# Optimization experiments

Measured on AMD Instinct MI355X. Metric: run time of the kernel, lower is better.

Reference implementation:

```python
import jax, jax.numpy as jnp
import numpy as np

N_NODES = 50000
N_EDGES = 800000
IN_FT = 256
OUT_FT = 128


def setup_inputs() -> dict:
    key = jax.random.key(0)
    k_seq, k_src, k_dst, k_val, k_w = jax.random.split(key, 5)
    seq = jax.random.normal(k_seq, (N_NODES, IN_FT), dtype=jnp.float32)
    edge_src = jax.random.randint(k_src, (N_EDGES,), 0, N_NODES, dtype=jnp.int64)
    edge_dst = jax.random.randint(k_dst, (N_EDGES,), 0, N_NODES, dtype=jnp.int64)
    edge_val = jax.random.uniform(k_val, (N_EDGES,), dtype=jnp.float32)
    # xavier_uniform for Linear(in_ft, out_ft): limit = sqrt(6/(in+out))
    limit = float(np.sqrt(6.0 / (IN_FT + OUT_FT)))
    W = jax.random.uniform(k_w, (OUT_FT, IN_FT), minval=-limit, maxval=limit, dtype=jnp.float32)
    bias = jnp.zeros((OUT_FT,), dtype=jnp.float32)
    prelu_a = jnp.full((1,), 0.25, dtype=jnp.float32)  # nn.PReLU default slope
    return {"seq": seq, "edge_src": edge_src, "edge_dst": edge_dst,
            "edge_val": edge_val, "W": W, "bias": bias, "prelu_a": prelu_a}


def reference(seq, edge_src, edge_dst, edge_val, W, bias, prelu_a):
    # seq_fts = fc(seq): [N, out_ft]
    seq_fts = jnp.einsum('ni,oi->no', seq, W)
    # sparse spmm: out[dst] += val * seq_fts[src]
    msgs = seq_fts[edge_src] * edge_val[:, None]          # [E, out_ft]
    out = jax.ops.segment_sum(msgs, edge_dst, num_segments=seq.shape[0])
    out = out + bias                                       # bias add
    # PReLU with learnable slope a
    return jnp.where(out >= 0, out, prelu_a * out)
```

## Files before the change

kernel.cpp:

```cpp
#include <hip/hip_runtime.h>
#include <hip/hip_bf16.h>

#define N_NODES 50000
#define N_EDGES 800000
#define IN_FT 256
#define OUT_FT 128

typedef __bf16 bf16;
typedef __attribute__((ext_vector_type(8))) __bf16 bf16x8;
typedef __attribute__((ext_vector_type(4))) __bf16 bf16x4;
typedef __attribute__((ext_vector_type(4))) float floatx4;

static __device__ inline unsigned short f2bf_bits(float f) {
    unsigned u = __float_as_uint(f);
    return (unsigned short)((u + 0x7FFFu + ((u >> 16) & 1u)) >> 16);
}

#define BKN 128
#define NBUCK 392
#define EPB 2048
#define NBLK_A ((N_EDGES + EPB - 1) / EPB)
#define CELL 32
#define SXCAP 2560
#define GM 128
#define GEMM_BLKS ((N_NODES + GM - 1) / GM)
#define WP 264
#define OP 136
#define SMEM_BYTES (128 * OP * 2 > 64 * WP * 2 ? 128 * OP * 2 : 64 * WP * 2)

template<int NTHREADS>
__device__ inline int blk_scan_incl(int v, int t, int* wsum) {
    const int lane = t & 63;
    const int w = t >> 6;
#pragma unroll
    for (int s = 1; s < 64; s <<= 1) {
        int o = __shfl_up(v, s, 64);
        if (lane >= s) v += o;
    }
    __syncthreads();
    if (lane == 63) wsum[w] = v;
    __syncthreads();
    if (w == 0) {
        constexpr int NWAVE = NTHREADS / 64;
        int x = (lane < NWAVE) ? wsum[lane] : 0;
#pragma unroll
        for (int s = 1; s < NWAVE; s <<= 1) {
            int o = __shfl_up(x, s, 64);
            if (lane >= s) x += o;
        }
        if (lane < NWAVE) wsum[lane] = x;
    }
    __syncthreads();
    return v + ((w > 0) ? wsum[w - 1] : 0);
}

__global__ __launch_bounds__(512, 6) void k_ga(const float* __restrict__ seq,
                                               const float* __restrict__ W,
                                               unsigned short* __restrict__ seq_fts,
                                               const int* __restrict__ src,
                                               const int* __restrict__ dst,
                                               const float* __restrict__ val,
                                               int* __restrict__ cnt,
                                               uint2* __restrict__ part) {
    const int t = threadIdx.x;
    __shared__ __align__(16) char smem[SMEM_BYTES];
    if (blockIdx.x < GEMM_BLKS) {
        bf16* Wlds = (bf16*)smem;
        const int lane = t & 63;
        const int wave = t >> 6;
        const int quad = lane >> 4;
        const int l16  = lane & 15;

        int arow = blockIdx.x * GM + wave * 16 + l16;
        if (arow >= N_NODES) arow = 0;
        const float* ap = seq + (size_t)arow * IN_FT + quad * 8;
        bf16x8 afr[8];
#pragma unroll
        for (int s = 0; s < 8; ++s) {
            float4 v0 = *(const float4*)(ap + s * 32);
            float4 v1 = *(const float4*)(ap + s * 32 + 4);
            bf16x8 a;
            a[0] = (bf16)v0.x; a[1] = (bf16)v0.y; a[2] = (bf16)v0.z; a[3] = (bf16)v0.w;
            a[4] = (bf16)v1.x; a[5] = (bf16)v1.y; a[6] = (bf16)v1.z; a[7] = (bf16)v1.w;
            afr[s] = a;
        }

        floatx4 acc[2][4];
#pragma unroll
        for (int h2 = 0; h2 < 2; ++h2)
#pragma unroll
            for (int q = 0; q < 4; ++q) acc[h2][q] = (floatx4){0.f, 0.f, 0.f, 0.f};

#pragma unroll
        for (int h2 = 0; h2 < 2; ++h2) {
            __syncthreads();
            {
                const int row = t >> 3;
                const int c0 = (t & 7) * 32;
                const float* wsrc = W + (size_t)(h2 * 64 + row) * IN_FT + c0;
                bf16* dstp = Wlds + row * WP + c0;
#pragma unroll
                for (int c = 0; c < 8; ++c) {
                    float4 vv = *(const float4*)(wsrc + c * 4);
                    bf16x4 o = {(bf16)vv.x, (bf16)vv.y, (bf16)vv.z, (bf16)vv.w};
                    *(bf16x4*)(dstp + c * 4) = o;
                }
            }
            __syncthreads();
#pragma unroll
            for (int s = 0; s < 8; ++s) {
#pragma unroll
                for (int q = 0; q < 4; ++q) {
                    bf16x8 bfr = *(const bf16x8*)(Wlds + (q * 16 + l16) * WP + quad * 8 + s * 32);
                    acc[h2][q] = __builtin_amdgcn_mfma_f32_16x16x32_bf16(afr[s], bfr, acc[h2][q], 0, 0, 0);
                }
            }
        }
        __syncthreads();
        unsigned short* olds = (unsigned short*)smem;
#pragma unroll
        for (int h2 = 0; h2 < 2; ++h2)
#pragma unroll
            for (int q = 0; q < 4; ++q) {
                const int col = (h2 * 4 + q) * 16 + l16;
#pragma unroll
                for (int r = 0; r < 4; ++r)
                    olds[(wave * 16 + quad * 4 + r) * OP + col] = f2bf_bits(acc[h2][q][r]);
            }
        __syncthreads();
        {
            const int lr0 = t >> 4;
            const int cseg = (t & 15) * 8;
            const int mb = blockIdx.x * GM;
#pragma unroll
            for (int it = 0; it < 4; ++it) {
                const int lr = it * 32 + lr0;
                const int m = mb + lr;
                if (m < N_NODES)
                    *(uint4*)(seq_fts + (size_t)m * OUT_FT + cseg) =
                        *(const uint4*)(olds + lr * OP + cseg);
            }
        }
    } else {
        int*   ib    = (int*)smem;
        int*   h     = ib;
        int*   lbase = ib + 392;
        int*   wsum  = ib + 784;
        int*   totp  = ib + 792;
        uint2* srt   = (uint2*)(smem + 3200);

        const int B2 = blockIdx.x - GEMM_BLKS;
        const int e0 = B2 * EPB;
        if (t < NBUCK) h[t] = 0;
        __syncthreads();

        int      myd[4];
        int      myofs[4];
        unsigned myx[4];
#pragma unroll
        for (int k = 0; k < 4; ++k) {
            int e = e0 + k * 512 + t;
            int d = (e < N_EDGES) ? dst[e] : -1;
            myd[k] = d;
            if (d >= 0) {
                myx[k] = (unsigned)(unsigned short)src[e]
                       | ((unsigned)f2bf_bits(val[e]) << 16);
                myofs[k] = atomicAdd(&h[d >> 7], 1);
            }
        }
        __syncthreads();
        const int v = (t < NBUCK) ? min(h[t], CELL) : 0;
        const int inc = blk_scan_incl<512>(v, t, wsum);
        if (t < NBUCK) { lbase[t] = inc - v; cnt[t * NBLK_A + B2] = v; }
        if (t == 511) *totp = inc;
        __syncthreads();
        const int total = *totp;
#pragma unroll
        for (int k = 0; k < 4; ++k) {
            int d = myd[k];
            if (d >= 0 && myofs[k] < CELL)
                srt[lbase[d >> 7] + myofs[k]] = make_uint2(myx[k], (unsigned)d);
        }
        __syncthreads();
        for (int i = t; i < total; i += 512) {
            uint2 r = srt[i];
            int bb = (int)(r.y >> 7);
            part[(size_t)(bb * NBLK_A + B2) * CELL + (unsigned)(i - lbase[bb])] = r;
        }
    }
}

#define NW 16
__global__ __launch_bounds__(1024) void k_BG(const int* __restrict__ cnt,
                                             const uint2* __restrict__ part,
                                             const unsigned* __restrict__ fts,
                                             const float* __restrict__ bias,
                                             const float* __restrict__ prelu_a,
                                             float* __restrict__ out) {
    const int b = blockIdx.x, t = threadIdx.x;
    __shared__ int wsum[16];
    __shared__ int tot_sh;
    __shared__ int ncnt[BKN], nbase[BKN], ncur[BKN];
    __shared__ unsigned fx[SXCAP];
    __shared__ unsigned char fdn[SXCAP];
    __shared__ unsigned sx[SXCAP];

    if (t < BKN) ncnt[t] = 0;
    const int len = (t < NBLK_A) ? cnt[b * NBLK_A + t] : 0;
    const int inc = blk_scan_incl<1024>(len, t, wsum);
    const int cellbase = inc - len;
    if (t == 1023) tot_sh = inc;
    __syncthreads();
    const int totc = (tot_sh < SXCAP) ? tot_sh : SXCAP;

    if (t < NBLK_A) {
        const uint2* cp = part + (size_t)(b * NBLK_A + t) * CELL;
        for (int k = 0; k < len; ++k) {
            int idx = cellbase + k;
            if (idx < SXCAP) {
                uint2 r = cp[k];
                int dn = (int)(r.y & (BKN - 1));
                fx[idx] = r.x;
                fdn[idx] = (unsigned char)dn;
                atomicAdd(&ncnt[dn], 1);
            }
        }
    }
    __syncthreads();
    const int v2 = (t < BKN) ? ncnt[t] : 0;
    const int inc2 = blk_scan_incl<1024>(v2, t, wsum);
    if (t < BKN) {
        nbase[t] = inc2 - v2;
        ncur[t]  = inc2 - v2;
    }
    __syncthreads();
    for (int i = t; i < totc; i += 1024) {
        unsigned x = fx[i];
        int dn = fdn[i];
        int j = atomicAdd(&ncur[dn], 1);
        sx[j] = x;
    }
    __syncthreads();

    const int wave = t >> 6;
    const int lane = t & 63;
    const float2 bb2 = *(const float2*)&bias[lane * 2];
    const float a = prelu_a[0];
    for (int ln = wave; ln < BKN; ln += NW) {
        const int n = b * BKN + ln;
        if (n >= N_NODES) continue;
        const int s0 = nbase[ln];
        const int s1 = s0 + ncnt[ln];
        float acc0 = 0.f, acc1 = 0.f;
        int j = s0;
        for (; j + 7 < s1; j += 8) {
            unsigned x0 = sx[j],     x1 = sx[j + 1];
            unsigned x2 = sx[j + 2], x3 = sx[j + 3];
            unsigned x4 = sx[j + 4], x5 = sx[j + 5];
            unsigned x6 = sx[j + 6], x7 = sx[j + 7];
            unsigned q0 = fts[(x0 & 0xFFFFu) * 64u + lane];
            unsigned q1 = fts[(x1 & 0xFFFFu) * 64u + lane];
            unsigned q2 = fts[(x2 & 0xFFFFu) * 64u + lane];
            unsigned q3 = fts[(x3 & 0xFFFFu) * 64u + lane];
            unsigned q4 = fts[(x4 & 0xFFFFu) * 64u + lane];
            unsigned q5 = fts[(x5 & 0xFFFFu) * 64u + lane];
            unsigned q6 = fts[(x6 & 0xFFFFu) * 64u + lane];
            unsigned q7 = fts[(x7 & 0xFFFFu) * 64u + lane];
            acc0 += __uint_as_float(x0 & 0xFFFF0000u) * __uint_as_float(q0 << 16);
            acc1 += __uint_as_float(x0 & 0xFFFF0000u) * __uint_as_float(q0 & 0xFFFF0000u);
            acc0 += __uint_as_float(x1 & 0xFFFF0000u) * __uint_as_float(q1 << 16);
            acc1 += __uint_as_float(x1 & 0xFFFF0000u) * __uint_as_float(q1 & 0xFFFF0000u);
            acc0 += __uint_as_float(x2 & 0xFFFF0000u) * __uint_as_float(q2 << 16);
            acc1 += __uint_as_float(x2 & 0xFFFF0000u) * __uint_as_float(q2 & 0xFFFF0000u);
            acc0 += __uint_as_float(x3 & 0xFFFF0000u) * __uint_as_float(q3 << 16);
            acc1 += __uint_as_float(x3 & 0xFFFF0000u) * __uint_as_float(q3 & 0xFFFF0000u);
            acc0 += __uint_as_float(x4 & 0xFFFF0000u) * __uint_as_float(q4 << 16);
            acc1 += __uint_as_float(x4 & 0xFFFF0000u) * __uint_as_float(q4 & 0xFFFF0000u);
            acc0 += __uint_as_float(x5 & 0xFFFF0000u) * __uint_as_float(q5 << 16);
            acc1 += __uint_as_float(x5 & 0xFFFF0000u) * __uint_as_float(q5 & 0xFFFF0000u);
            acc0 += __uint_as_float(x6 & 0xFFFF0000u) * __uint_as_float(q6 << 16);
            acc1 += __uint_as_float(x6 & 0xFFFF0000u) * __uint_as_float(q6 & 0xFFFF0000u);
            acc0 += __uint_as_float(x7 & 0xFFFF0000u) * __uint_as_float(q7 << 16);
            acc1 += __uint_as_float(x7 & 0xFFFF0000u) * __uint_as_float(q7 & 0xFFFF0000u);
        }
        for (; j + 3 < s1; j += 4) {
            unsigned x0 = sx[j],     x1 = sx[j + 1];
            unsigned x2 = sx[j + 2], x3 = sx[j + 3];
            unsigned q0 = fts[(x0 & 0xFFFFu) * 64u + lane];
            unsigned q1 = fts[(x1 & 0xFFFFu) * 64u + lane];
            unsigned q2 = fts[(x2 & 0xFFFFu) * 64u + lane];
            unsigned q3 = fts[(x3 & 0xFFFFu) * 64u + lane];
            acc0 += __uint_as_float(x0 & 0xFFFF0000u) * __uint_as_float(q0 << 16);
            acc1 += __uint_as_float(x0 & 0xFFFF0000u) * __uint_as_float(q0 & 0xFFFF0000u);
            acc0 += __uint_as_float(x1 & 0xFFFF0000u) * __uint_as_float(q1 << 16);
            acc1 += __uint_as_float(x1 & 0xFFFF0000u) * __uint_as_float(q1 & 0xFFFF0000u);
            acc0 += __uint_as_float(x2 & 0xFFFF0000u) * __uint_as_float(q2 << 16);
            acc1 += __uint_as_float(x2 & 0xFFFF0000u) * __uint_as_float(q2 & 0xFFFF0000u);
            acc0 += __uint_as_float(x3 & 0xFFFF0000u) * __uint_as_float(q3 << 16);
            acc1 += __uint_as_float(x3 & 0xFFFF0000u) * __uint_as_float(q3 & 0xFFFF0000u);
        }
        for (; j < s1; ++j) {
            unsigned x0 = sx[j];
            unsigned q0 = fts[(x0 & 0xFFFFu) * 64u + lane];
            float v0 = __uint_as_float(x0 & 0xFFFF0000u);
            acc0 += v0 * __uint_as_float(q0 << 16);
            acc1 += v0 * __uint_as_float(q0 & 0xFFFF0000u);
        }
        float x0f = acc0 + bb2.x;
        float x1f = acc1 + bb2.y;
        x0f = (x0f >= 0.f) ? x0f : a * x0f;
        x1f = (x1f >= 0.f) ? x1f : a * x1f;
        *(float2*)&out[(size_t)n * OUT_FT + lane * 2] = make_float2(x0f, x1f);
    }
}

extern "C" void kernel_launch(void* const* d_in, const int* in_sizes, int n_in,
                              void* d_out, int out_size, void* d_ws, size_t ws_size,
                              hipStream_t stream) {
    const float* seq      = (const float*)d_in[0];
    const int*   edge_src = (const int*)d_in[1];
    const int*   edge_dst = (const int*)d_in[2];
    const float* edge_val = (const float*)d_in[3];
    const float* W        = (const float*)d_in[4];
    const float* bias     = (const float*)d_in[5];
    const float* prelu_a  = (const float*)d_in[6];
    float* out = (float*)d_out;

    char* ws = (char*)d_ws;
    size_t off = 0;
    auto alloc = [&](size_t bytes) {
        void* p = ws + off;
        off = (off + bytes + 255) & ~(size_t)255;
        return p;
    };
    unsigned short* seq_fts = (unsigned short*)alloc((size_t)N_NODES * OUT_FT * sizeof(unsigned short));
    int*   cnt  = (int*)alloc((size_t)NBUCK * NBLK_A * sizeof(int));
    uint2* part = (uint2*)alloc((size_t)NBUCK * NBLK_A * CELL * sizeof(uint2));
    (void)ws_size; (void)in_sizes; (void)n_in; (void)out_size;

    k_ga<<<GEMM_BLKS + NBLK_A, 512, 0, stream>>>(seq, W, seq_fts,
                                                 edge_src, edge_dst, edge_val,
                                                 cnt, part);
    k_BG<<<NBUCK, 1024, 0, stream>>>(cnt, part, (const unsigned*)seq_fts,
                                     bias, prelu_a, out);
}
```

Before: 152.6 us.

## Interleave GEMM and edge-bucketing blocks and issue W load before A-fragment loads

```diff
diff --git a/kernel.cpp b/kernel.cpp
--- a/kernel.cpp
+++ b/kernel.cpp
@@ -64,14 +64,28 @@
                                                uint2* __restrict__ part) {
     const int t = threadIdx.x;
     __shared__ __align__(16) char smem[SMEM_BYTES];
-    if (blockIdx.x < GEMM_BLKS) {
+    const int bid = blockIdx.x >> 1;
+    if ((blockIdx.x & 1) == 0) {
         bf16* Wlds = (bf16*)smem;
         const int lane = t & 63;
         const int wave = t >> 6;
         const int quad = lane >> 4;
         const int l16  = lane & 15;
 
-        int arow = blockIdx.x * GM + wave * 16 + l16;
+        {
+            const int row = t >> 3;
+            const int c0 = (t & 7) * 32;
+            const float* wsrc = W + (size_t)row * IN_FT + c0;
+            bf16* dstp = Wlds + row * WP + c0;
+#pragma unroll
+            for (int c = 0; c < 8; ++c) {
+                float4 vv = *(const float4*)(wsrc + c * 4);
+                bf16x4 o = {(bf16)vv.x, (bf16)vv.y, (bf16)vv.z, (bf16)vv.w};
+                *(bf16x4*)(dstp + c * 4) = o;
+            }
+        }
+
+        int arow = bid * GM + wave * 16 + l16;
         if (arow >= N_NODES) arow = 0;
         const float* ap = seq + (size_t)arow * IN_FT + quad * 8;
         bf16x8 afr[8];
@@ -91,29 +105,35 @@
 #pragma unroll
             for (int q = 0; q < 4; ++q) acc[h2][q] = (floatx4){0.f, 0.f, 0.f, 0.f};
 
-#pragma unroll
-        for (int h2 = 0; h2 < 2; ++h2) {
-            __syncthreads();
-            {
-                const int row = t >> 3;
-                const int c0 = (t & 7) * 32;
-                const float* wsrc = W + (size_t)(h2 * 64 + row) * IN_FT + c0;
-                bf16* dstp = Wlds + row * WP + c0;
-#pragma unroll
-                for (int c = 0; c < 8; ++c) {
-                    float4 vv = *(const float4*)(wsrc + c * 4);
-                    bf16x4 o = {(bf16)vv.x, (bf16)vv.y, (bf16)vv.z, (bf16)vv.w};
-                    *(bf16x4*)(dstp + c * 4) = o;
-                }
-            }
-            __syncthreads();
-#pragma unroll
-            for (int s = 0; s < 8; ++s) {
-#pragma unroll
-                for (int q = 0; q < 4; ++q) {
-                    bf16x8 bfr = *(const bf16x8*)(Wlds + (q * 16 + l16) * WP + quad * 8 + s * 32);
-                    acc[h2][q] = __builtin_amdgcn_mfma_f32_16x16x32_bf16(afr[s], bfr, acc[h2][q], 0, 0, 0);
-                }
+        __syncthreads();
+#pragma unroll
+        for (int s = 0; s < 8; ++s) {
+#pragma unroll
+            for (int q = 0; q < 4; ++q) {
+                bf16x8 bfr = *(const bf16x8*)(Wlds + (q * 16 + l16) * WP + quad * 8 + s * 32);
+                acc[0][q] = __builtin_amdgcn_mfma_f32_16x16x32_bf16(afr[s], bfr, acc[0][q], 0, 0, 0);
+            }
+        }
+        __syncthreads();
+        {
+            const int row = t >> 3;
+            const int c0 = (t & 7) * 32;
+            const float* wsrc = W + (size_t)(64 + row) * IN_FT + c0;
+            bf16* dstp = Wlds + row * WP + c0;
+#pragma unroll
+            for (int c = 0; c < 8; ++c) {
+                float4 vv = *(const float4*)(wsrc + c * 4);
+                bf16x4 o = {(bf16)vv.x, (bf16)vv.y, (bf16)vv.z, (bf16)vv.w};
+                *(bf16x4*)(dstp + c * 4) = o;
+            }
+        }
+        __syncthreads();
+#pragma unroll
+        for (int s = 0; s < 8; ++s) {
+#pragma unroll
+            for (int q = 0; q < 4; ++q) {
+                bf16x8 bfr = *(const bf16x8*)(Wlds + (q * 16 + l16) * WP + quad * 8 + s * 32);
+                acc[1][q] = __builtin_amdgcn_mfma_f32_16x16x32_bf16(afr[s], bfr, acc[1][q], 0, 0, 0);
             }
         }
         __syncthreads();
@@ -131,7 +151,7 @@
         {
             const int lr0 = t >> 4;
             const int cseg = (t & 15) * 8;
-            const int mb = blockIdx.x * GM;
+            const int mb = bid * GM;
 #pragma unroll
             for (int it = 0; it < 4; ++it) {
                 const int lr = it * 32 + lr0;
@@ -149,7 +169,7 @@
         int*   totp  = ib + 792;
         uint2* srt   = (uint2*)(smem + 3200);
 
-        const int B2 = blockIdx.x - GEMM_BLKS;
+        const int B2 = bid;
         const int e0 = B2 * EPB;
         if (t < NBUCK) h[t] = 0;
         __syncthreads();
```

Result: slower. 168.0 us (+10.1%).
